# Optimization experiments

Hardware: AMD Instinct MI355X
Metric: run time of the kernel (lower is better)

The kernel has to match this reference:

```python
import jax, jax.numpy as jnp
import numpy as np
import math

B, S, D = 2, 4096, 1024

def setup_inputs() -> dict:
    key = jax.random.key(0)
    ks = jax.random.split(key, 8)
    s = 1.0 / math.sqrt(D)
    return {
        "x": jax.random.normal(ks[0], (B, S, D), dtype=jnp.float32),
        "Wq": jax.random.normal(ks[1], (D, D), dtype=jnp.float32) * s,
        "bq": jax.random.normal(ks[2], (D,), dtype=jnp.float32) * s,
        "Wk": jax.random.normal(ks[3], (D, D), dtype=jnp.float32) * s,
        "bk": jax.random.normal(ks[4], (D,), dtype=jnp.float32) * s,
        "Wv": jax.random.normal(ks[5], (D, D), dtype=jnp.float32) * s,
        "bv": jax.random.normal(ks[6], (D,), dtype=jnp.float32) * s,
        "phase_bias": jnp.zeros((D,), dtype=jnp.float32),
    }

def reference(x, Wq, bq, Wk, bk, Wv, bv, phase_bias):
    d = x.shape[-1]
    # buffer: wavelengths = arange(1, d+1) * 2*pi/d
    wavelengths = jnp.arange(1, d + 1, dtype=jnp.float32) * (2.0 * math.pi / d)
    inv_wl = 1.0 / (wavelengths + 1e-8)
    # torch Linear: x @ W.T + b
    Q = jnp.einsum('bsd,ed->bse', x, Wq) + bq
    K = jnp.einsum('bsd,ed->bse', x, Wk) + bk
    V = jnp.einsum('bsd,ed->bse', x, Wv) + bv
    theta_q = Q * inv_wl + phase_bias
    theta_k = K * inv_wl + phase_bias
    # cos(a)cos(b) + sin(a)sin(b) summed over feature dim
    sim = (jnp.einsum('bsd,btd->bst', jnp.cos(theta_q), jnp.cos(theta_k))
           + jnp.einsum('bsd,btd->bst', jnp.sin(theta_q), jnp.sin(theta_k)))
    weights = jax.nn.softmax(sim / math.sqrt(d), axis=-1)
    return jnp.einsum('bst,btd->bsd', weights, V)
```

## Files before the change

### kernel.cpp

```cpp
#include <hip/hip_runtime.h>
#include <math.h>


typedef __attribute__((ext_vector_type(8))) short bf16x8;
typedef __attribute__((ext_vector_type(4))) float f32x4;

__device__ __forceinline__ float b2f(unsigned short h) {
    union { unsigned int u; float f; } v; v.u = ((unsigned int)h) << 16; return v.f;
}
__device__ __forceinline__ unsigned short f2b(float f) {
    union { float f; unsigned int u; } v; v.f = f;
    unsigned int r = v.u + 0x7fffu + ((v.u >> 16) & 1u);
    return (unsigned short)(r >> 16);
}

__device__ __forceinline__ void async_load16(const unsigned short* g, unsigned short* l) {
    __builtin_amdgcn_global_load_lds(
        (const __attribute__((address_space(1))) unsigned int*)g,
        (__attribute__((address_space(3))) unsigned int*)l, 16, 0, 0);
}

__device__ __forceinline__ void fast_sincos(float th, float* sn, float* cs) {
    float rev = th * 0.15915494309189535f;
    float fr  = rev - floorf(rev);
    float s, c;
    asm("v_sin_f32 %0, %1" : "=v"(s) : "v"(fr));
    asm("v_cos_f32 %0, %1" : "=v"(c) : "v"(fr));
    *sn = s; *cs = c;
}

__global__ __launch_bounds__(256) void split_kernel(
    const float* __restrict__ src,
    unsigned short* __restrict__ hi, unsigned short* __restrict__ lo, int n4)
{
    int i = blockIdx.x * 256 + threadIdx.x;
    if (i >= n4) return;
    float4 v = ((const float4*)src)[i];
    float f[4] = { v.x, v.y, v.z, v.w };
    unsigned short h[4], l[4];
#pragma unroll
    for (int j = 0; j < 4; j++) {
        h[j] = f2b(f[j]);
        float r = f[j] - b2f(h[j]);
        l[j] = f2b(r);
    }
    uint2 ho, lv;
    ho.x = (unsigned int)h[0] | ((unsigned int)h[1] << 16);
    ho.y = (unsigned int)h[2] | ((unsigned int)h[3] << 16);
    lv.x = (unsigned int)l[0] | ((unsigned int)l[1] << 16);
    lv.y = (unsigned int)l[2] | ((unsigned int)l[3] << 16);
    ((uint2*)hi)[i] = ho;
    ((uint2*)lo)[i] = lv;
}

__global__ __launch_bounds__(256) void split_w_kernel(
    const float* __restrict__ Wq, const float* __restrict__ Wk,
    const float* __restrict__ Wv,
    unsigned short* __restrict__ hi, unsigned short* __restrict__ lo)
{
    const int y = blockIdx.y;
    const float* src = (y == 0) ? Wq : ((y == 1) ? Wk : Wv);
    size_t off4 = (size_t)y * (1024 * 1024 / 4);
    int i = blockIdx.x * 256 + threadIdx.x;
    float4 v = ((const float4*)src)[i];
    float f[4] = { v.x, v.y, v.z, v.w };
    unsigned short h[4], l[4];
#pragma unroll
    for (int j = 0; j < 4; j++) {
        h[j] = f2b(f[j]);
        float r = f[j] - b2f(h[j]);
        l[j] = f2b(r);
    }
    uint2 ho, lv;
    ho.x = (unsigned int)h[0] | ((unsigned int)h[1] << 16);
    ho.y = (unsigned int)h[2] | ((unsigned int)h[3] << 16);
    lv.x = (unsigned int)l[0] | ((unsigned int)l[1] << 16);
    lv.y = (unsigned int)l[2] | ((unsigned int)l[3] << 16);
    ((uint2*)hi)[off4 + i] = ho;
    ((uint2*)lo)[off4 + i] = lv;
}

__global__ __launch_bounds__(256, 3) void proj_kernel(
    const unsigned short* __restrict__ Xhi, const unsigned short* __restrict__ Xlo,
    const unsigned short* __restrict__ Whi, const unsigned short* __restrict__ Wlo,
    const float* __restrict__ bq, const float* __restrict__ bk,
    const float* __restrict__ bv, const float* __restrict__ phase,
    unsigned short* __restrict__ Qf, unsigned short* __restrict__ Kf,
    unsigned short* __restrict__ Vt)
{
    const int m0 = blockIdx.y * 128;
    const int n0 = blockIdx.x * 128;

    __shared__ unsigned short Ah[128 * 32], Al[128 * 32];
    __shared__ unsigned short Bh[128 * 32], Bl[128 * 32];

    const int tid  = threadIdx.x;
    const int lane = tid & 63;
    const int w    = tid >> 6;
    const int wr   = w >> 1, wc = w & 1;
    const int l15  = lane & 15, q = lane >> 4;
    const int qx   = q ^ ((l15 >> 1) & 3);

    f32x4 acc[4][4];
#pragma unroll
    for (int a = 0; a < 4; a++)
#pragma unroll
        for (int b = 0; b < 4; b++) acc[a][b] = (f32x4){0.f, 0.f, 0.f, 0.f};

    for (int k0 = 0; k0 < 1024; k0 += 32) {
#pragma unroll
        for (int i = 0; i < 2; i++) {
            int idx = tid + 256 * i;
            int row = idx >> 2;
            int cc  = idx & 3;
            int scc = cc ^ ((row >> 1) & 3);
            size_t ga = (size_t)(m0 + row) * 1024 + k0 + cc * 8;
            size_t gb = (size_t)(n0 + row) * 1024 + k0 + cc * 8;
            *(uint4*)&Ah[(row * 4 + scc) * 8] = *(const uint4*)&Xhi[ga];
            *(uint4*)&Al[(row * 4 + scc) * 8] = *(const uint4*)&Xlo[ga];
            *(uint4*)&Bh[(row * 4 + scc) * 8] = *(const uint4*)&Whi[gb];
            *(uint4*)&Bl[(row * 4 + scc) * 8] = *(const uint4*)&Wlo[gb];
        }
        __syncthreads();
        bf16x8 ah[4], al[4];
#pragma unroll
        for (int mt = 0; mt < 4; mt++) {
            int off = ((wr * 64 + mt * 16 + l15) * 4 + qx) * 8;
            ah[mt] = *(const bf16x8*)&Ah[off];
            al[mt] = *(const bf16x8*)&Al[off];
        }
#pragma unroll
        for (int nt = 0; nt < 4; nt++) {
            int off = ((wc * 64 + nt * 16 + l15) * 4 + qx) * 8;
            bf16x8 bh = *(const bf16x8*)&Bh[off];
            bf16x8 bl = *(const bf16x8*)&Bl[off];
#pragma unroll
            for (int mt = 0; mt < 4; mt++) {
                acc[mt][nt] = __builtin_amdgcn_mfma_f32_16x16x32_bf16(
                    ah[mt], bh, acc[mt][nt], 0, 0, 0);
                acc[mt][nt] = __builtin_amdgcn_mfma_f32_16x16x32_bf16(
                    ah[mt], bl, acc[mt][nt], 0, 0, 0);
                acc[mt][nt] = __builtin_amdgcn_mfma_f32_16x16x32_bf16(
                    al[mt], bh, acc[mt][nt], 0, 0, 0);
            }
        }
        __syncthreads();
    }

    const int z = n0 >> 10;
    const float* bias = (z == 0) ? bq : ((z == 1) ? bk : bv);
    const float w0 = (float)(2.0 * M_PI / 1024.0);

#pragma unroll
    for (int mt = 0; mt < 4; mt++) {
#pragma unroll
        for (int nt = 0; nt < 4; nt++) {
            int n = n0 + wc * 64 + nt * 16 + l15;
            int f = n & 1023;
            float bsv = bias[f];
            float wl  = (float)(f + 1) * w0;
            float inv = 1.0f / (wl + 1e-8f);
            float phv = phase[f];
#pragma unroll
            for (int r = 0; r < 4; r++) {
                int m  = m0 + wr * 64 + mt * 16 + q * 4 + r;
                int bb = m >> 12;
                int s  = m & 4095;
                float val = acc[mt][nt][r] + bsv;
                if (z == 2) {
                    Vt[((size_t)bb * 1024 + f) * 4096 + s] = f2b(val);
                } else {
                    float th = fmaf(val, inv, phv);
                    float sn, cs;
                    fast_sincos(th, &sn, &cs);
                    unsigned short* dst = (z == 0) ? Qf : Kf;
                    size_t base = ((size_t)bb * 4096 + s) * 2048;
                    dst[base + f]        = f2b(cs);
                    dst[base + 1024 + f] = f2b(sn);
                }
            }
        }
    }
}

template <int LDA, int LDB, int LDC, int KLEN, int SLICES, bool ATOMIC, bool PARTIAL>
__device__ __forceinline__ void gemm_core(
    const unsigned short* __restrict__ A,
    const unsigned short* __restrict__ Bm,
    float* __restrict__ C, size_t sA, size_t sB, size_t sC)
{
    const int bz = blockIdx.z;
    const int batch = bz / SLICES;
    const int slice = bz % SLICES;
    A  += (size_t)batch * sA;
    Bm += (size_t)batch * sB;
    C  += PARTIAL ? (size_t)bz * sC : (size_t)batch * sC;
    const int koff = slice * KLEN;

    const int m0 = blockIdx.y * 128;
    const int n0 = blockIdx.x * 128;

    __shared__ unsigned short As[128 * 32];
    __shared__ unsigned short Bs[128 * 32];

    const int tid  = threadIdx.x;
    const int lane = tid & 63;
    const int w    = tid >> 6;
    const int wr   = w >> 1, wc = w & 1;
    const int l15  = lane & 15, q = lane >> 4;
    const int lrow = lane >> 2;
    const int cgl  = (lane & 3) ^ ((lane >> 3) & 3);
    const int qx   = q ^ ((l15 >> 1) & 3);

    f32x4 acc[4][4];
#pragma unroll
    for (int a = 0; a < 4; a++)
#pragma unroll
        for (int b = 0; b < 4; b++) acc[a][b] = (f32x4){0.f, 0.f, 0.f, 0.f};

    for (int k0 = 0; k0 < KLEN; k0 += 32) {
        int kg = koff + k0;
#pragma unroll
        for (int i = 0; i < 2; i++) {
            int chunk = w * 2 + i;
            async_load16(&A[(size_t)(m0 + chunk * 16 + lrow) * LDA + kg + cgl * 8],
                         &As[chunk * 512]);
            async_load16(&Bm[(size_t)(n0 + chunk * 16 + lrow) * LDB + kg + cgl * 8],
                         &Bs[chunk * 512]);
        }
        __syncthreads();
        bf16x8 af[4], bfr[4];
#pragma unroll
        for (int mt = 0; mt < 4; mt++) {
            int ar = wr * 64 + mt * 16 + l15;
            af[mt] = *(const bf16x8*)&As[(ar * 4 + qx) * 8];
        }
#pragma unroll
        for (int nt = 0; nt < 4; nt++) {
            int br = wc * 64 + nt * 16 + l15;
            bfr[nt] = *(const bf16x8*)&Bs[(br * 4 + qx) * 8];
        }
#pragma unroll
        for (int mt = 0; mt < 4; mt++)
#pragma unroll
            for (int nt = 0; nt < 4; nt++)
                acc[mt][nt] = __builtin_amdgcn_mfma_f32_16x16x32_bf16(
                    af[mt], bfr[nt], acc[mt][nt], 0, 0, 0);
        __syncthreads();
    }

#pragma unroll
    for (int mt = 0; mt < 4; mt++) {
#pragma unroll
        for (int nt = 0; nt < 4; nt++) {
            int n = n0 + wc * 64 + nt * 16 + l15;
#pragma unroll
            for (int r = 0; r < 4; r++) {
                int m = m0 + wr * 64 + mt * 16 + q * 4 + r;
                float* p = &C[(size_t)m * LDC + n];
                if (ATOMIC)
                    __hip_atomic_fetch_add(p, acc[mt][nt][r],
                                           __ATOMIC_RELAXED, __HIP_MEMORY_SCOPE_AGENT);
                else
                    *p = acc[mt][nt][r];
            }
        }
    }
}

__global__ __launch_bounds__(256) void k4_gemm_atomic(
    const unsigned short* __restrict__ A, const unsigned short* __restrict__ Bm,
    float* __restrict__ C, size_t sA, size_t sB, size_t sC)
{
    gemm_core<8192, 4096, 1024, 1024, 4, true, false>(A, Bm, C, sA, sB, sC);
}

template <int GX, int LDA, int LDB, int LDC, int KLEN, int SLICES, bool PARTIAL>
__device__ __forceinline__ void gemm256_core(
    const unsigned short* __restrict__ A,
    const unsigned short* __restrict__ Bm,
    float* __restrict__ C, size_t sA, size_t sB, size_t sC)
{
    const int bz = blockIdx.z;
    const int batch = bz / SLICES;
    const int slice = bz % SLICES;
    A  += (size_t)batch * sA;
    Bm += (size_t)batch * sB;
    C  += PARTIAL ? (size_t)bz * sC : (size_t)batch * sC;
    const int koff = slice * KLEN;

    const int nwg = GX * 16;
    const int lin = blockIdx.x + GX * blockIdx.y;
    const int nb  = (lin & 7) * (nwg >> 3) + (lin >> 3);
    const int m0 = (nb / GX) * 256;
    const int n0 = (nb % GX) * 256;

    __shared__ unsigned short lds[4 * 16384];

    const int tid  = threadIdx.x;
    const int lane = tid & 63;
    const int wid  = tid >> 6;
    const int wm   = wid >> 2;
    const int wn   = wid & 3;
    const int l15  = lane & 15, q = lane >> 4;
    const int lrow = lane >> 2;
    const int cgl  = (lane & 3) ^ ((lane >> 3) & 3);
    const int qx   = q ^ ((l15 >> 1) & 3);

    f32x4 acc[8][4];
#pragma unroll
    for (int a = 0; a < 8; a++)
#pragma unroll
        for (int b = 0; b < 4; b++) acc[a][b] = (f32x4){0.f, 0.f, 0.f, 0.f};

    const int NT = KLEN / 32;

    const int c0 = (wid * 2 + 0) * 512;
    const int c1 = (wid * 2 + 1) * 512;
    const unsigned short* aS0 = &A[(size_t)(m0 + (wid * 2 + 0) * 16 + lrow) * LDA + koff + cgl * 8];
    const unsigned short* aS1 = &A[(size_t)(m0 + (wid * 2 + 1) * 16 + lrow) * LDA + koff + cgl * 8];
    const unsigned short* bS0 = &Bm[(size_t)(n0 + (wid * 2 + 0) * 16 + lrow) * LDB + koff + cgl * 8];
    const unsigned short* bS1 = &Bm[(size_t)(n0 + (wid * 2 + 1) * 16 + lrow) * LDB + koff + cgl * 8];

    auto STAGE_A = [&](int kt) {
        unsigned short* buf = &lds[(kt & 3) * 16384];
        async_load16(aS0 + (size_t)kt * 32, &buf[c0]);
        async_load16(aS1 + (size_t)kt * 32, &buf[c1]);
    };
    auto STAGE_B = [&](int kt) {
        unsigned short* buf = &lds[(kt & 3) * 16384];
        async_load16(bS0 + (size_t)kt * 32, &buf[8192 + c0]);
        async_load16(bS1 + (size_t)kt * 32, &buf[8192 + c1]);
    };

    auto ITER = [&](int t, bool doStage, int vm) {
        const unsigned short* buf = &lds[(t & 3) * 16384];
        bf16x8 af[8], bfr[4];
#pragma unroll
        for (int mt = 0; mt < 8; mt++)
            af[mt] = *(const bf16x8*)&buf[((wm * 128 + mt * 16 + l15) * 4 + qx) * 8];
#pragma unroll
        for (int nt = 0; nt < 2; nt++)
            bfr[nt] = *(const bf16x8*)&buf[8192 + ((wn * 64 + nt * 16 + l15) * 4 + qx) * 8];
        if (doStage) STAGE_A(t + 3);
        asm volatile("s_barrier" ::: "memory");
        asm volatile("s_waitcnt lgkmcnt(0)" ::: "memory");
        __builtin_amdgcn_s_setprio(1);
#pragma unroll
        for (int mt = 0; mt < 8; mt++)
#pragma unroll
            for (int nt = 0; nt < 2; nt++)
                acc[mt][nt] = __builtin_amdgcn_mfma_f32_16x16x32_bf16(
                    af[mt], bfr[nt], acc[mt][nt], 0, 0, 0);
        __builtin_amdgcn_s_setprio(0);
        asm volatile("s_barrier" ::: "memory");
#pragma unroll
        for (int nt = 2; nt < 4; nt++)
            bfr[nt] = *(const bf16x8*)&buf[8192 + ((wn * 64 + nt * 16 + l15) * 4 + qx) * 8];
        if (doStage) STAGE_B(t + 3);
        asm volatile("s_barrier" ::: "memory");
        asm volatile("s_waitcnt lgkmcnt(0)" ::: "memory");
        __builtin_amdgcn_s_setprio(1);
#pragma unroll
        for (int mt = 0; mt < 8; mt++)
#pragma unroll
            for (int nt = 2; nt < 4; nt++)
                acc[mt][nt] = __builtin_amdgcn_mfma_f32_16x16x32_bf16(
                    af[mt], bfr[nt], acc[mt][nt], 0, 0, 0);
        __builtin_amdgcn_s_setprio(0);
        if (vm == 8)      asm volatile("s_waitcnt vmcnt(8)" ::: "memory");
        else if (vm == 4) asm volatile("s_waitcnt vmcnt(4)" ::: "memory");
        else if (vm == 0) asm volatile("s_waitcnt vmcnt(0)" ::: "memory");
        asm volatile("s_barrier" ::: "memory");
    };

    STAGE_A(0); STAGE_B(0);
    STAGE_A(1); STAGE_B(1);
    STAGE_A(2); STAGE_B(2);
    asm volatile("s_waitcnt vmcnt(8)" ::: "memory");
    asm volatile("s_barrier" ::: "memory");

    for (int t = 0; t < NT - 3; ++t)
        ITER(t, true, 8);
    ITER(NT - 3, false, 4);
    ITER(NT - 2, false, 0);
    ITER(NT - 1, false, -1);

#pragma unroll
    for (int mt = 0; mt < 8; mt++) {
#pragma unroll
        for (int nt = 0; nt < 4; nt++) {
            const int n = n0 + wn * 64 + nt * 16 + l15;
#pragma unroll
            for (int r = 0; r < 4; r++) {
                const int m = m0 + wm * 128 + mt * 16 + q * 4 + r;
                C[(size_t)m * LDC + n] = acc[mt][nt][r];
            }
        }
    }
}

__global__ __launch_bounds__(512, 2) void k2_gemm256(
    const unsigned short* __restrict__ A, const unsigned short* __restrict__ Bm,
    float* __restrict__ C, size_t sA, size_t sB, size_t sC)
{
    gemm256_core<16, 2048, 2048, 4096, 2048, 1, false>(A, Bm, C, sA, sB, sC);
}

__global__ __launch_bounds__(512, 2) void k4_gemm256(
    const unsigned short* __restrict__ A, const unsigned short* __restrict__ Bm,
    float* __restrict__ C, size_t sA, size_t sB, size_t sC)
{
    gemm256_core<4, 8192, 4096, 1024, 2048, 2, true>(A, Bm, C, sA, sB, sC);
}

__global__ __launch_bounds__(256) void reduce_kernel(
    const float* __restrict__ part, float* __restrict__ out)
{
    int j4 = blockIdx.x * 256 + threadIdx.x;
    int b  = j4 >> 20;
    int jj = j4 & 1048575;
    const float4* p0 = (const float4*)(part + (size_t)(b * 2 + 0) * 4194304);
    const float4* p1 = (const float4*)(part + (size_t)(b * 2 + 1) * 4194304);
    float4 a = p0[jj], c = p1[jj];
    float4 r; r.x = a.x + c.x; r.y = a.y + c.y; r.z = a.z + c.z; r.w = a.w + c.w;
    ((float4*)out)[j4] = r;
}

__global__ __launch_bounds__(256) void softmax_kernel(float* __restrict__ simbase,
                                                      size_t batchStride)
{
    const int row = blockIdx.x;
    float* sim = simbase + (size_t)(row >> 12) * batchStride;
    const int r = row & 4095;
    const float* pin = sim + (size_t)r * 4096;
    unsigned short* pout = (unsigned short*)sim + (size_t)r * 8192;
    const int tid = threadIdx.x;

    float v[16];
#pragma unroll
    for (int i = 0; i < 4; i++) {
        float4 d = ((const float4*)pin)[tid * 4 + i];
        v[4 * i + 0] = d.x * 0.03125f;
        v[4 * i + 1] = d.y * 0.03125f;
        v[4 * i + 2] = d.z * 0.03125f;
        v[4 * i + 3] = d.w * 0.03125f;
    }

    float m = v[0];
#pragma unroll
    for (int i = 1; i < 16; i++) m = fmaxf(m, v[i]);
    for (int o = 32; o > 0; o >>= 1) m = fmaxf(m, __shfl_xor(m, o));
    __shared__ float red[4];
    if ((tid & 63) == 0) red[tid >> 6] = m;
    __syncthreads();
    m = fmaxf(fmaxf(red[0], red[1]), fmaxf(red[2], red[3]));
    __syncthreads();

    float e[16];
    float s = 0.f;
#pragma unroll
    for (int i = 0; i < 16; i++) { e[i] = expf(v[i] - m); s += e[i]; }
    for (int o = 32; o > 0; o >>= 1) s += __shfl_xor(s, o);
    if ((tid & 63) == 0) red[tid >> 6] = s;
    __syncthreads();
    float l = (red[0] + red[1]) + (red[2] + red[3]);
    float inv = 1.0f / l;

#pragma unroll
    for (int c = 0; c < 2; c++) {
        unsigned int wds[4];
#pragma unroll
        for (int i = 0; i < 4; i++) {
            unsigned int lo = f2b(e[c * 8 + 2 * i] * inv);
            unsigned int hi = f2b(e[c * 8 + 2 * i + 1] * inv);
            wds[i] = lo | (hi << 16);
        }
        uint4 o4; o4.x = wds[0]; o4.y = wds[1]; o4.z = wds[2]; o4.w = wds[3];
        ((uint4*)pout)[tid * 2 + c] = o4;
    }
}

extern "C" void kernel_launch(void* const* d_in, const int* in_sizes, int n_in,
                              void* d_out, int out_size, void* d_ws, size_t ws_size,
                              hipStream_t stream)
{
    const float* x  = (const float*)d_in[0];
    const float* Wq = (const float*)d_in[1];
    const float* bq = (const float*)d_in[2];
    const float* Wk = (const float*)d_in[3];
    const float* bk = (const float*)d_in[4];
    const float* Wv = (const float*)d_in[5];
    const float* bv = (const float*)d_in[6];
    const float* ph = (const float*)d_in[7];

    char* ws = (char*)d_ws;
    const size_t SIMB = (size_t)4096 * 4096 * 4;
    unsigned short* Xhi = (unsigned short*)ws;
    unsigned short* Xlo = Xhi + (size_t)8192 * 1024;
    unsigned short* Whi = Xlo + (size_t)8192 * 1024;
    unsigned short* Wlo = Whi + (size_t)3072 * 1024;
    float*          sim0 = (float*)ws;
    unsigned short* Qf = (unsigned short*)(ws + SIMB);
    unsigned short* Kf = Qf + (size_t)2 * 4096 * 2048;
    unsigned short* Vt = Kf + (size_t)2 * 4096 * 2048;
    float*          sim1 = (float*)(ws + SIMB + (size_t)83886080);
    float*          part = (float*)(ws + SIMB);
    const bool twoSim = ws_size >= (size_t)218103808;

    split_kernel<<<8192, 256, 0, stream>>>(x, Xhi, Xlo, 8192 * 1024 / 4);
    split_w_kernel<<<dim3(1024, 3), 256, 0, stream>>>(Wq, Wk, Wv, Whi, Wlo);
    proj_kernel<<<dim3(24, 64), 256, 0, stream>>>(Xhi, Xlo, Whi, Wlo,
                                                  bq, bk, bv, ph, Qf, Kf, Vt);

    const size_t sQK = (size_t)4096 * 2048;
    const size_t sV  = (size_t)1024 * 4096;
    const size_t sO  = (size_t)4096 * 1024;

    if (twoSim) {
        const size_t sSim = (size_t)(sim1 - sim0);
        k2_gemm256<<<dim3(16, 16, 2), 512, 0, stream>>>(Qf, Kf, sim0, sQK, sQK, sSim);
        softmax_kernel<<<8192, 256, 0, stream>>>(sim0, sSim);
        k4_gemm256<<<dim3(4, 16, 4), 512, 0, stream>>>((const unsigned short*)sim0, Vt,
                                                       part, sSim * 2, sV, sO);
        reduce_kernel<<<8192, 256, 0, stream>>>(part, (float*)d_out);
    } else {
        hipMemsetAsync(d_out, 0, (size_t)2 * 4096 * 1024 * sizeof(float), stream);
        for (int b = 0; b < 2; b++) {
            const unsigned short* Qb = Qf + (size_t)b * sQK;
            const unsigned short* Kb = Kf + (size_t)b * sQK;
            const unsigned short* Vb = Vt + (size_t)b * sV;
            float* outb = (float*)d_out + (size_t)b * sO;
            k2_gemm256<<<dim3(16, 16, 1), 512, 0, stream>>>(Qb, Kb, sim0, 0, 0, 0);
            softmax_kernel<<<4096, 256, 0, stream>>>(sim0, 0);
            k4_gemm_atomic<<<dim3(8, 32, 4), 256, 0, stream>>>(
                (const unsigned short*)sim0, Vb, outb, 0, 0, 0);
        }
    }
}
```

Before: 507.9 us.

## Restructure projection GEMM with triple-buffered async LDS loads and larger tiles

The QKV projection kernel moves from a 128x128 tile with 4 waves and synchronous global-to-LDS copies to a 256x128 tile with 8 waves. It uses a 3-stage ring of LDS buffers filled by global_load_lds async copies issued two k-steps ahead. The split-bf16 MFMA work is interleaved in three phases with barriers and priority hints so loads overlap compute. This aims to hide global memory latency and raise MFMA utilisation in the projection stage, at the cost of much more LDS per block (about 144 KB), lower occupancy, and more fragile hand-written waitcnt/barrier synchronisation.

Result: no change. 503.9 us (-0.8%).

```diff
diff --git a/kernel.cpp b/kernel.cpp
--- a/kernel.cpp
+++ b/kernel.cpp
@@ -80,7 +80,7 @@
     ((uint2*)lo)[off4 + i] = lv;
 }
 
-__global__ __launch_bounds__(256, 3) void proj_kernel(
+__global__ __launch_bounds__(512, 2) void proj_kernel(
     const unsigned short* __restrict__ Xhi, const unsigned short* __restrict__ Xlo,
     const unsigned short* __restrict__ Whi, const unsigned short* __restrict__ Wlo,
     const float* __restrict__ bq, const float* __restrict__ bk,
@@ -88,84 +88,140 @@
     unsigned short* __restrict__ Qf, unsigned short* __restrict__ Kf,
     unsigned short* __restrict__ Vt)
 {
-    const int m0 = blockIdx.y * 128;
+    const int m0 = blockIdx.y * 256;
     const int n0 = blockIdx.x * 128;
 
-    __shared__ unsigned short Ah[128 * 32], Al[128 * 32];
-    __shared__ unsigned short Bh[128 * 32], Bl[128 * 32];
+    __shared__ unsigned short lds[3 * 24576];
 
     const int tid  = threadIdx.x;
     const int lane = tid & 63;
-    const int w    = tid >> 6;
-    const int wr   = w >> 1, wc = w & 1;
+    const int wid  = tid >> 6;
+    const int wm   = wid >> 2;
+    const int wn   = wid & 3;
     const int l15  = lane & 15, q = lane >> 4;
+    const int lrow = lane >> 2;
+    const int cgl  = (lane & 3) ^ ((lane >> 3) & 3);
     const int qx   = q ^ ((l15 >> 1) & 3);
 
-    f32x4 acc[4][4];
-#pragma unroll
-    for (int a = 0; a < 4; a++)
-#pragma unroll
-        for (int b = 0; b < 4; b++) acc[a][b] = (f32x4){0.f, 0.f, 0.f, 0.f};
-
-    for (int k0 = 0; k0 < 1024; k0 += 32) {
-#pragma unroll
-        for (int i = 0; i < 2; i++) {
-            int idx = tid + 256 * i;
-            int row = idx >> 2;
-            int cc  = idx & 3;
-            int scc = cc ^ ((row >> 1) & 3);
-            size_t ga = (size_t)(m0 + row) * 1024 + k0 + cc * 8;
-            size_t gb = (size_t)(n0 + row) * 1024 + k0 + cc * 8;
-            *(uint4*)&Ah[(row * 4 + scc) * 8] = *(const uint4*)&Xhi[ga];
-            *(uint4*)&Al[(row * 4 + scc) * 8] = *(const uint4*)&Xlo[ga];
-            *(uint4*)&Bh[(row * 4 + scc) * 8] = *(const uint4*)&Whi[gb];
-            *(uint4*)&Bl[(row * 4 + scc) * 8] = *(const uint4*)&Wlo[gb];
-        }
-        __syncthreads();
-        bf16x8 ah[4], al[4];
-#pragma unroll
-        for (int mt = 0; mt < 4; mt++) {
-            int off = ((wr * 64 + mt * 16 + l15) * 4 + qx) * 8;
-            ah[mt] = *(const bf16x8*)&Ah[off];
-            al[mt] = *(const bf16x8*)&Al[off];
-        }
-#pragma unroll
-        for (int nt = 0; nt < 4; nt++) {
-            int off = ((wc * 64 + nt * 16 + l15) * 4 + qx) * 8;
-            bf16x8 bh = *(const bf16x8*)&Bh[off];
-            bf16x8 bl = *(const bf16x8*)&Bl[off];
-#pragma unroll
-            for (int mt = 0; mt < 4; mt++) {
+    const unsigned short* gsrc[6];
+    int loff[6];
+#pragma unroll
+    for (int i = 0; i < 6; i++) {
+        int c = wid * 6 + i;
+        const unsigned short* sp; int row; int off;
+        if (c < 16)      { sp = Xhi; row = m0 + c * 16;         off = c * 512; }
+        else if (c < 32) { sp = Xlo; row = m0 + (c - 16) * 16;  off = 8192 + (c - 16) * 512; }
+        else if (c < 40) { sp = Whi; row = n0 + (c - 32) * 16;  off = 16384 + (c - 32) * 512; }
+        else             { sp = Wlo; row = n0 + (c - 40) * 16;  off = 20480 + (c - 40) * 512; }
+        gsrc[i] = sp + (size_t)(row + lrow) * 1024 + cgl * 8;
+        loff[i] = off;
+    }
+
+    f32x4 acc[8][2];
+#pragma unroll
+    for (int a = 0; a < 8; a++)
+#pragma unroll
+        for (int b = 0; b < 2; b++) acc[a][b] = (f32x4){0.f, 0.f, 0.f, 0.f};
+
+    const int NT = 32;
+
+    auto STAGE2 = [&](int kt, int bufi, int i0) {
+        unsigned short* buf = &lds[bufi * 24576];
+#pragma unroll
+        for (int j = 0; j < 2; j++)
+            async_load16(gsrc[i0 + j] + kt * 32, &buf[loff[i0 + j]]);
+    };
+
+    auto ITER = [&](int t, int bc, int bs, bool doStage, int vm) {
+        const unsigned short* buf = &lds[bc * 24576];
+        bf16x8 ah[8], al[8], bh[2], bl[2];
+#pragma unroll
+        for (int mt = 0; mt < 8; mt++)
+            ah[mt] = *(const bf16x8*)&buf[((wm * 128 + mt * 16 + l15) * 4 + qx) * 8];
+#pragma unroll
+        for (int nt = 0; nt < 2; nt++)
+            bh[nt] = *(const bf16x8*)&buf[16384 + ((wn * 32 + nt * 16 + l15) * 4 + qx) * 8];
+        if (doStage) STAGE2(t + 2, bs, 0);
+        asm volatile("s_barrier" ::: "memory");
+        asm volatile("s_waitcnt lgkmcnt(0)" ::: "memory");
+        __builtin_amdgcn_s_setprio(1);
+#pragma unroll
+        for (int mt = 0; mt < 8; mt++)
+#pragma unroll
+            for (int nt = 0; nt < 2; nt++)
                 acc[mt][nt] = __builtin_amdgcn_mfma_f32_16x16x32_bf16(
-                    ah[mt], bh, acc[mt][nt], 0, 0, 0);
+                    ah[mt], bh[nt], acc[mt][nt], 0, 0, 0);
+        __builtin_amdgcn_s_setprio(0);
+        asm volatile("s_barrier" ::: "memory");
+#pragma unroll
+        for (int nt = 0; nt < 2; nt++)
+            bl[nt] = *(const bf16x8*)&buf[20480 + ((wn * 32 + nt * 16 + l15) * 4 + qx) * 8];
+        if (doStage) STAGE2(t + 2, bs, 2);
+        asm volatile("s_barrier" ::: "memory");
+        asm volatile("s_waitcnt lgkmcnt(0)" ::: "memory");
+        __builtin_amdgcn_s_setprio(1);
+#pragma unroll
+        for (int mt = 0; mt < 8; mt++)
+#pragma unroll
+            for (int nt = 0; nt < 2; nt++)
                 acc[mt][nt] = __builtin_amdgcn_mfma_f32_16x16x32_bf16(
-                    ah[mt], bl, acc[mt][nt], 0, 0, 0);
+                    ah[mt], bl[nt], acc[mt][nt], 0, 0, 0);
+        __builtin_amdgcn_s_setprio(0);
+        asm volatile("s_barrier" ::: "memory");
+#pragma unroll
+        for (int mt = 0; mt < 8; mt++)
+            al[mt] = *(const bf16x8*)&buf[8192 + ((wm * 128 + mt * 16 + l15) * 4 + qx) * 8];
+        if (doStage) STAGE2(t + 2, bs, 4);
+        asm volatile("s_barrier" ::: "memory");
+        asm volatile("s_waitcnt lgkmcnt(0)" ::: "memory");
+        __builtin_amdgcn_s_setprio(1);
+#pragma unroll
+        for (int mt = 0; mt < 8; mt++)
+#pragma unroll
+            for (int nt = 0; nt < 2; nt++)
                 acc[mt][nt] = __builtin_amdgcn_mfma_f32_16x16x32_bf16(
-                    al[mt], bh, acc[mt][nt], 0, 0, 0);
-            }
-        }
-        __syncthreads();
-    }
-
-    const int z = n0 >> 10;
+                    al[mt], bh[nt], acc[mt][nt], 0, 0, 0);
+        __builtin_amdgcn_s_setprio(0);
+        if (vm == 6)      asm volatile("s_waitcnt vmcnt(6)" ::: "memory");
+        else if (vm == 0) asm volatile("s_waitcnt vmcnt(0)" ::: "memory");
+        asm volatile("s_barrier" ::: "memory");
+    };
+
+    STAGE2(0, 0, 0); STAGE2(0, 0, 2); STAGE2(0, 0, 4);
+    STAGE2(1, 1, 0); STAGE2(1, 1, 2); STAGE2(1, 1, 4);
+    asm volatile("s_waitcnt vmcnt(6)" ::: "memory");
+    asm volatile("s_barrier" ::: "memory");
+
+    int bc = 0, bs = 2;
+    for (int t = 0; t < NT - 2; ++t) {
+        ITER(t, bc, bs, true, 6);
+        bc = (bc == 2) ? 0 : bc + 1;
+        bs = (bs == 2) ? 0 : bs + 1;
+    }
+    ITER(NT - 2, bc, 0, false, 0);
+    bc = (bc == 2) ? 0 : bc + 1;
+    ITER(NT - 1, bc, 0, false, -1);
+
+    const int z = blockIdx.x >> 3;
     const float* bias = (z == 0) ? bq : ((z == 1) ? bk : bv);
     const float w0 = (float)(2.0 * M_PI / 1024.0);
 
 #pragma unroll
-    for (int mt = 0; mt < 4; mt++) {
-#pragma unroll
-        for (int nt = 0; nt < 4; nt++) {
-            int n = n0 + wc * 64 + nt * 16 + l15;
-            int f = n & 1023;
-            float bsv = bias[f];
-            float wl  = (float)(f + 1) * w0;
-            float inv = 1.0f / (wl + 1e-8f);
-            float phv = phase[f];
+    for (int nt = 0; nt < 2; nt++) {
+        const int n  = n0 + wn * 32 + nt * 16 + l15;
+        const int f  = n & 1023;
+        const float bsv = bias[f];
+        const float wl  = (float)(f + 1) * w0;
+        const float inv = 1.0f / (wl + 1e-8f);
+        const float phv = phase[f];
+        unsigned short* dst = (z == 0) ? Qf : Kf;
+#pragma unroll
+        for (int mt = 0; mt < 8; mt++) {
 #pragma unroll
             for (int r = 0; r < 4; r++) {
-                int m  = m0 + wr * 64 + mt * 16 + q * 4 + r;
-                int bb = m >> 12;
-                int s  = m & 4095;
+                const int m  = m0 + wm * 128 + mt * 16 + q * 4 + r;
+                const int bb = m >> 12;
+                const int s  = m & 4095;
                 float val = acc[mt][nt][r] + bsv;
                 if (z == 2) {
                     Vt[((size_t)bb * 1024 + f) * 4096 + s] = f2b(val);
@@ -173,7 +229,6 @@
                     float th = fmaf(val, inv, phv);
                     float sn, cs;
                     fast_sincos(th, &sn, &cs);
-                    unsigned short* dst = (z == 0) ? Qf : Kf;
                     size_t base = ((size_t)bb * 4096 + s) * 2048;
                     dst[base + f]        = f2b(cs);
                     dst[base + 1024 + f] = f2b(sn);
@@ -510,7 +565,7 @@
 
     split_kernel<<<8192, 256, 0, stream>>>(x, Xhi, Xlo, 8192 * 1024 / 4);
     split_w_kernel<<<dim3(1024, 3), 256, 0, stream>>>(Wq, Wk, Wv, Whi, Wlo);
-    proj_kernel<<<dim3(24, 64), 256, 0, stream>>>(Xhi, Xlo, Whi, Wlo,
+    proj_kernel<<<dim3(24, 32), 512, 0, stream>>>(Xhi, Xlo, Whi, Wlo,
                                                   bq, bk, bv, ph, Qf, Kf, Vt);
 
     const size_t sQK = (size_t)4096 * 2048;
```
